# Kernel tuning notes

Measured on AMD Instinct MI355X. Metric: run time of the kernel, lower is better.

Reference implementation:

```python
import jax, jax.numpy as jnp
import numpy as np

B, IN, H, D, C, K = 4096, 128, 256, 32, 8, 256
HS = D // 2  # structure_filter hidden (latent_dim > 2)
EPS = 1e-6
MAX_NORM = 0.99


def _gelu(t):
    return jax.nn.gelu(t, approximate=False)  # torch nn.GELU default = exact erf


def _project_to_ball(z):
    norm = jnp.maximum(jnp.linalg.norm(z, axis=-1, keepdims=True), EPS)
    scale = jnp.minimum(MAX_NORM / norm, 1.0)
    return z * scale


def _hyperbolic_distance(xp, yp):
    # Poincare-ball distance: arccosh(1 + 2*|x-y|^2 / ((1-|x|^2)(1-|y|^2)))
    sq = jnp.sum((xp - yp) ** 2, axis=-1)
    xn = jnp.sum(xp * xp, axis=-1)
    yn = jnp.sum(yp * yp, axis=-1)
    denom = jnp.maximum((1.0 - xn) * (1.0 - yn), EPS)
    arg = jnp.maximum(1.0 + 2.0 * sq / denom, 1.0 + EPS)
    return jnp.arccosh(arg)


def setup_inputs() -> dict:
    key = jax.random.key(0)
    ks = jax.random.split(key, 14)
    n = lambda k, shape, s: (jax.random.normal(k, shape, dtype=jnp.float32) * s)
    centers = jax.random.normal(ks[7], (C, D), dtype=jnp.float32)
    centers = centers / jnp.maximum(jnp.linalg.norm(centers, axis=-1, keepdims=True), EPS)
    return {
        "x": jax.random.normal(ks[0], (B, IN), dtype=jnp.float32),
        "W1": n(ks[1], (IN, H), 0.05), "b1": jnp.zeros((H,), jnp.float32),
        "W2": n(ks[2], (H, H), 0.05), "b2": jnp.zeros((H,), jnp.float32),
        "Wv": n(ks[3], (H, D), 0.05), "bv": jnp.zeros((D,), jnp.float32),
        "centers": centers,
        "codebook": n(ks[8], (C, K, D), 0.02),
        "Ws1": n(ks[9], (D, HS), 0.1), "bs1": jnp.zeros((HS,), jnp.float32),
        "Ws2": n(ks[10], (HS, D), 0.1), "bs2": jnp.zeros((D,), jnp.float32),
    }


def reference(x, W1, b1, W2, b2, Wv, bv, centers, codebook, Ws1, bs1, Ws2, bs2):
    sg = jax.lax.stop_gradient
    feats = _gelu(_gelu(x @ W1 + b1) @ W2 + b2)          # [B,H]
    v = feats @ Wv + bv                                   # [B,D]
    scores = (v @ centers.T) / jnp.sqrt(jnp.asarray(D, v.dtype))
    router = jax.nn.softmax(scores, axis=-1)              # [B,C]
    K_chart = jnp.argmax(router, axis=1)                  # [B]
    c_bar = router @ centers                              # [B,D]
    v_local = v - c_bar                                   # [B,D]
    diff = v_local[:, None, None, :] - codebook[None]     # [B,C,K,D]
    dist = jnp.sum(diff * diff, axis=-1)                  # [B,C,K]
    indices = jnp.argmin(dist, axis=-1)                   # [B,C]
    z_q_all = codebook[jnp.arange(C)[None, :], indices]   # [B,C,D]
    v_bc = jnp.broadcast_to(v_local[:, None, :], z_q_all.shape)
    v_proj = _project_to_ball(v_bc)
    w_det = sg(router)
    d_cb = _hyperbolic_distance(z_q_all, sg(v_proj))      # [B,C]
    codebook_loss = jnp.sum(jnp.mean(d_cb ** 2 * w_det, axis=0))
    d_cm = _hyperbolic_distance(sg(z_q_all), v_proj)
    commitment = jnp.sum(jnp.mean(d_cm ** 2 * w_det, axis=0))
    vq_loss = codebook_loss + 0.25 * commitment
    z_q_blended = jnp.sum(z_q_all * router[..., None], axis=1)  # [B,D]
    K_code = jnp.take_along_axis(indices, K_chart[:, None], axis=1)[:, 0]
    delta = v_local[:, None, :] - sg(z_q_all)             # [B,C,D]
    z_n_all = _gelu(delta @ Ws1 + bs1) @ Ws2 + bs2        # [B,C,D]
    z_n = jnp.sum(z_n_all * router[..., None], axis=1)    # [B,D]
    z_tex = (v_local - sg(z_q_blended)) - z_n
    z_q_st = v_local + sg(z_q_blended - v_local)
    z_geo = c_bar + z_q_st + z_n
    return (K_chart, K_code, z_n, z_tex, router, z_geo, vq_loss, indices, z_n_all, c_bar, v_local)
```

## Files before the change

### kernel.cpp

```cpp
#include <hip/hip_runtime.h>
#include <math.h>

#define NB 4096
#define NIN 128
#define NH 256
#define ND 32
#define NC 8
#define NK 256
#define NHS 16

#define OFF_KCHART 0
#define OFF_KCODE  4096
#define OFF_ZN     8192
#define OFF_ZTEX   (OFF_ZN + 4096*32)
#define OFF_ROUTER (OFF_ZTEX + 4096*32)
#define OFF_ZGEO   (OFF_ROUTER + 4096*8)
#define OFF_LOSS   (OFF_ZGEO + 4096*32)
#define OFF_IND    (OFF_LOSS + 1)
#define OFF_ZNALL  (OFF_IND + 4096*8)
#define OFF_CBAR   (OFF_ZNALL + 4096*8*32)
#define OFF_VLOC   (OFF_CBAR + 4096*32)

__device__ __forceinline__ float gelu_exact(float x) {
    return x * (erff(x / 1.41421356237309504f) + 1.0f) * 0.5f;
}

template<int K>
__global__ __launch_bounds__(256)
void gemm_bias_gelu(const float* __restrict__ A, const float* __restrict__ W,
                    const float* __restrict__ bias, float* __restrict__ out) {
    const int N = 256;
    __shared__ float sB[2][32][68];
    const int t  = threadIdx.x;
    const int n0 = blockIdx.x * 64;
    const int r0 = blockIdx.y * 32;
    const int ty = t >> 4, tx = t & 15;
    const int bk = t >> 4, bc = t & 15;

    float4 bias4 = *(const float4*)(bias + n0 + tx * 4);

    float4 pb0 = *(const float4*)(W + bk * N + n0 + bc * 4);
    float4 pb1 = *(const float4*)(W + (bk + 16) * N + n0 + bc * 4);

    const float* Ab0 = A + (r0 + ty * 2 + 0) * K;
    const float* Ab1 = A + (r0 + ty * 2 + 1) * K;
    float ac[2][4], an[2][4];
    {
        float4 c0 = *(const float4*)(Ab0 + 0), c1 = *(const float4*)(Ab1 + 0);
        ac[0][0]=c0.x; ac[0][1]=c0.y; ac[0][2]=c0.z; ac[0][3]=c0.w;
        ac[1][0]=c1.x; ac[1][1]=c1.y; ac[1][2]=c1.z; ac[1][3]=c1.w;
        float4 d0 = *(const float4*)(Ab0 + 4), d1 = *(const float4*)(Ab1 + 4);
        an[0][0]=d0.x; an[0][1]=d0.y; an[0][2]=d0.z; an[0][3]=d0.w;
        an[1][0]=d1.x; an[1][1]=d1.y; an[1][2]=d1.z; an[1][3]=d1.w;
    }

    float acc[2][4];
    #pragma unroll
    for (int i = 0; i < 2; i++)
        #pragma unroll
        for (int j = 0; j < 4; j++) acc[i][j] = 0.f;

    int buf = 0;
    for (int kk = 0; kk < K; kk += 32) {
        *(float4*)(&sB[buf][bk][bc*4])    = pb0;
        *(float4*)(&sB[buf][bk+16][bc*4]) = pb1;
        __syncthreads();
        if (kk + 32 < K) {
            pb0 = *(const float4*)(W + (kk + 32 + bk) * N + n0 + bc * 4);
            pb1 = *(const float4*)(W + (kk + 32 + bk + 16) * N + n0 + bc * 4);
        }
        #pragma unroll
        for (int c = 0; c < 8; c++) {
            int knext = kk + (c + 2) * 4;
            if (knext > K - 4) knext = K - 4;
            float4 p0 = *(const float4*)(Ab0 + knext);
            float4 p1 = *(const float4*)(Ab1 + knext);
            #pragma unroll
            for (int u = 0; u < 4; u++) {
                float4 bv = *(const float4*)(&sB[buf][c * 4 + u][tx * 4]);
                float bb[4] = {bv.x, bv.y, bv.z, bv.w};
                #pragma unroll
                for (int j = 0; j < 4; j++) {
                    acc[0][j] = fmaf(ac[0][u], bb[j], acc[0][j]);
                    acc[1][j] = fmaf(ac[1][u], bb[j], acc[1][j]);
                }
            }
            #pragma unroll
            for (int u = 0; u < 4; u++) { ac[0][u] = an[0][u]; ac[1][u] = an[1][u]; }
            an[0][0]=p0.x; an[0][1]=p0.y; an[0][2]=p0.z; an[0][3]=p0.w;
            an[1][0]=p1.x; an[1][1]=p1.y; an[1][2]=p1.z; an[1][3]=p1.w;
        }
        buf ^= 1;
    }
    float bb4[4] = {bias4.x, bias4.y, bias4.z, bias4.w};
    #pragma unroll
    for (int i = 0; i < 2; i++) {
        int row = r0 + ty * 2 + i;
        float4 o;
        float* op = (float*)&o;
        #pragma unroll
        for (int j = 0; j < 4; j++) op[j] = gelu_exact(acc[i][j] + bb4[j]);
        *(float4*)(out + row * N + n0 + tx * 4) = o;
    }
}

__global__ __launch_bounds__(256)
void router_kernel(const float* __restrict__ feats, const float* __restrict__ Wv,
                   const float* __restrict__ bv, const float* __restrict__ centers,
                   float* __restrict__ out, float* __restrict__ vloc_ws) {
    __shared__ float sWvT[ND][260];
    __shared__ float sCent[NC * ND];
    __shared__ float sV[8][ND + 2];
    __shared__ float sScore[8][NC];
    __shared__ float sRout[8][NC];
    const int t = threadIdx.x;
    const int row0 = blockIdx.x * 8;
    {
        #pragma unroll
        for (int q = 0; q < 8; q++) {
            int id = t + q * 256;
            int k = id >> 3, c4 = (id & 7) * 4;
            float4 w = ((const float4*)Wv)[id];
            sWvT[c4 + 0][k] = w.x;
            sWvT[c4 + 1][k] = w.y;
            sWvT[c4 + 2][k] = w.z;
            sWvT[c4 + 3][k] = w.w;
        }
        if (t < 64) ((float4*)sCent)[t] = ((const float4*)centers)[t];
    }
    __syncthreads();
    const int r = t >> 5, cp = t & 31;
    const int row = row0 + r;
    float a0 = bv[cp];
    const float4* f4 = (const float4*)(feats + row * NH);
    for (int k4 = 0; k4 < NH / 4; k4++) {
        float4 f = f4[k4];
        float4 w = *(const float4*)(&sWvT[cp][k4 * 4]);
        a0 = fmaf(f.x, w.x, a0);
        a0 = fmaf(f.y, w.y, a0);
        a0 = fmaf(f.z, w.z, a0);
        a0 = fmaf(f.w, w.w, a0);
    }
    sV[r][cp] = a0;
    __syncthreads();
    if (t < 64) {
        int rr = t >> 3, c = t & 7;
        float s = 0.f;
        #pragma unroll
        for (int k = 0; k < ND; k++) s = fmaf(sV[rr][k], sCent[c * ND + k], s);
        sScore[rr][c] = s / 5.65685424949238f;
    }
    __syncthreads();
    if (t < 8) {
        const int rr = t, grow = row0 + rr;
        float sc[NC];
        float m = -3.4e38f; int kmax = 0;
        #pragma unroll
        for (int c = 0; c < NC; c++) {
            float s = sScore[rr][c];
            sc[c] = s;
            if (s > m) { m = s; kmax = c; }
        }
        float ssum = 0.f;
        #pragma unroll
        for (int c = 0; c < NC; c++) { float e = expf(sc[c] - m); sc[c] = e; ssum += e; }
        float inv = 1.f / ssum;
        #pragma unroll
        for (int c = 0; c < NC; c++) {
            float rv = sc[c] * inv;
            sRout[rr][c] = rv;
            out[OFF_ROUTER + grow * NC + c] = rv;
        }
        out[OFF_KCHART + grow] = (float)kmax;
    }
    __syncthreads();
    {
        const int col = cp;
        float cb = 0.f;
        #pragma unroll
        for (int c = 0; c < NC; c++) cb = fmaf(sRout[r][c], sCent[c * ND + col], cb);
        float vl = sV[r][col] - cb;
        out[OFF_CBAR + row * ND + col] = cb;
        out[OFF_VLOC + row * ND + col] = vl;
        vloc_ws[row * ND + col] = vl;
    }
}

__global__ __launch_bounds__(256)
void vq_chart(const float* __restrict__ codebook, const float* __restrict__ vloc_ws,
              const float* __restrict__ Ws1, const float* __restrict__ bs1,
              const float* __restrict__ Ws2, const float* __restrict__ bs2,
              float* __restrict__ out, float* __restrict__ loss_partial) {
    __shared__ float sCB[NK][36];
    __shared__ float sEn2[NK];
    __shared__ float sV[64][36];
    __shared__ float sBest[8][64];
    __shared__ int   sBidx[8][64];
    __shared__ int   sSel[64];
    __shared__ float sRoutv[64];
    __shared__ float sPscale[64];
    __shared__ float sLossArr[64];
    __shared__ float sWs1[ND][17];
    __shared__ float sWs2[NHS][33];
    __shared__ float sbs1[NHS], sbs2v[ND];
    const int t = threadIdx.x;
    const int c = blockIdx.x & 7;
    const int row0 = (blockIdx.x >> 3) * 64;

    {
        const float4* src = (const float4*)(codebook + c * NK * ND);
        #pragma unroll
        for (int q = 0; q < 8; q++) {
            int id = t + q * 256;
            int code = id >> 3, kq = (id & 7) * 4;
            *(float4*)(&sCB[code][kq]) = src[id];
        }
        #pragma unroll
        for (int q = 0; q < 2; q++) {
            int id = t + q * 256;
            int rr = id >> 3, kq = (id & 7) * 4;
            *(float4*)(&sV[rr][kq]) = ((const float4*)(vloc_ws + row0 * ND))[id];
        }
    }
    if (t < 128) {
        float4 w = ((const float4*)Ws1)[t];
        int k = t >> 2, o = (t & 3) * 4;
        sWs1[k][o] = w.x; sWs1[k][o+1] = w.y; sWs1[k][o+2] = w.z; sWs1[k][o+3] = w.w;
    } else {
        int u = t - 128;
        float4 w = ((const float4*)Ws2)[u];
        int k = u >> 3, o = (u & 7) * 4;
        sWs2[k][o] = w.x; sWs2[k][o+1] = w.y; sWs2[k][o+2] = w.z; sWs2[k][o+3] = w.w;
    }
    if (t < NHS) sbs1[t] = bs1[t];
    else if (t < NHS + ND) sbs2v[t - NHS] = bs2[t - NHS];
    if (t < 64) sRoutv[t] = out[OFF_ROUTER + (row0 + t) * NC + c];
    __syncthreads();
    {
        float s = 0.f;
        #pragma unroll
        for (int q = 0; q < 8; q++) {
            float4 e = *(const float4*)(&sCB[t][q * 4]);
            s = fmaf(e.x, e.x, s); s = fmaf(e.y, e.y, s);
            s = fmaf(e.z, e.z, s); s = fmaf(e.w, e.w, s);
        }
        sEn2[t] = s;
    }
    __syncthreads();

    const int r = t & 31, g = t >> 5;
    float vl0[ND], vl1[ND];
    #pragma unroll
    for (int q = 0; q < 8; q++) {
        float4 a = *(const float4*)(&sV[r][q * 4]);
        vl0[q*4] = a.x; vl0[q*4+1] = a.y; vl0[q*4+2] = a.z; vl0[q*4+3] = a.w;
        float4 b = *(const float4*)(&sV[r + 32][q * 4]);
        vl1[q*4] = b.x; vl1[q*4+1] = b.y; vl1[q*4+2] = b.z; vl1[q*4+3] = b.w;
    }
    float best0 = 3.4e38f, best1 = 3.4e38f;
    int bi0 = 0, bi1 = 0;
    for (int j = 0; j < 32; j++) {
        const int code = g * 32 + j;
        float dot0 = 0.f, dot1 = 0.f;
        #pragma unroll
        for (int q = 0; q < 8; q++) {
            float4 e = *(const float4*)(&sCB[code][q * 4]);
            dot0 = fmaf(vl0[q*4+0], e.x, dot0); dot1 = fmaf(vl1[q*4+0], e.x, dot1);
            dot0 = fmaf(vl0[q*4+1], e.y, dot0); dot1 = fmaf(vl1[q*4+1], e.y, dot1);
            dot0 = fmaf(vl0[q*4+2], e.z, dot0); dot1 = fmaf(vl1[q*4+2], e.z, dot1);
            dot0 = fmaf(vl0[q*4+3], e.w, dot0); dot1 = fmaf(vl1[q*4+3], e.w, dot1);
        }
        const float en2 = sEn2[code];
        float d0 = en2 - 2.f * dot0;
        float d1 = en2 - 2.f * dot1;
        if (d0 < best0) { best0 = d0; bi0 = code; }
        if (d1 < best1) { best1 = d1; bi1 = code; }
    }
    sBest[g][r] = best0;      sBidx[g][r] = bi0;
    sBest[g][r + 32] = best1; sBidx[g][r + 32] = bi1;
    __syncthreads();
    if (t < 64) {
        float bb = sBest[0][t]; int ii = sBidx[0][t];
        #pragma unroll
        for (int gg = 1; gg < 8; gg++) {
            float v = sBest[gg][t];
            if (v < bb) { bb = v; ii = sBidx[gg][t]; }
        }
        sSel[t] = ii;
        out[OFF_IND + (row0 + t) * NC + c] = (float)ii;
        float vn2 = 0.f;
        #pragma unroll
        for (int k = 0; k < ND; k++) { float v = sV[t][k]; vn2 = fmaf(v, v, vn2); }
        float norm = fmaxf(sqrtf(vn2), 1e-6f);
        sPscale[t] = fminf(0.99f / norm, 1.0f);
    }
    __syncthreads();

    const int i = t & 15, r16 = t >> 4;
    const float b1r = sbs1[i];
    const float bo0 = sbs2v[2*i], bo1 = sbs2v[2*i+1];
    #pragma unroll
    for (int pass = 0; pass < 4; pass++) {
        const int lrow = pass * 16 + r16;
        const int grow = row0 + lrow;
        const int sel = sSel[lrow];
        const float rc = sRoutv[lrow];
        const float ps = sPscale[lrow];
        float acc1 = b1r;
        #pragma unroll
        for (int k = 0; k < ND; k++) {
            float dlt = sV[lrow][k] - sCB[sel][k];
            acc1 = fmaf(dlt, sWs1[k][i], acc1);
        }
        float h = gelu_exact(acc1);
        float a0 = bo0, a1 = bo1;
        #pragma unroll
        for (int k = 0; k < NHS; k++) {
            float s1k = __shfl(h, k, 16);
            a0 = fmaf(s1k, sWs2[k][2*i],   a0);
            a1 = fmaf(s1k, sWs2[k][2*i+1], a1);
        }
        out[OFF_ZNALL + (grow * NC + c) * ND + 2*i]     = a0;
        out[OFF_ZNALL + (grow * NC + c) * ND + 2*i + 1] = a1;
        const float e0 = sCB[sel][2*i], e1 = sCB[sel][2*i+1];
        float yp0 = sV[lrow][2*i] * ps, yp1 = sV[lrow][2*i+1] * ps;
        float d0 = e0 - yp0, d1 = e1 - yp1;
        float sq = fmaf(d0, d0, d1 * d1);
        float xn = fmaf(e0, e0, e1 * e1);
        float yn = fmaf(yp0, yp0, yp1 * yp1);
        #pragma unroll
        for (int m = 1; m < 16; m <<= 1) {
            sq += __shfl_xor(sq, m, 16);
            xn += __shfl_xor(xn, m, 16);
            yn += __shfl_xor(yn, m, 16);
        }
        if (i == 0) {
            float denom = fmaxf((1.f - xn) * (1.f - yn), 1e-6f);
            float arg = fmaxf(1.f + 2.f * sq / denom, 1.f + 1e-6f);
            float dd = acoshf(arg);
            sLossArr[lrow] = dd * dd * rc;
        }
    }
    __syncthreads();
    if (t < 64) {
        float v = sLossArr[t];
        #pragma unroll
        for (int off = 32; off > 0; off >>= 1) v += __shfl_down(v, off, 64);
        if (t == 0) loss_partial[blockIdx.x] = v;
    }
}

__global__ __launch_bounds__(256)
void finalize2_kernel(const float* __restrict__ codebook, const float* __restrict__ vloc_ws,
                      float* __restrict__ out, const float* __restrict__ partials) {
    const int gid = blockIdx.x * 256 + threadIdx.x;
    const int row = gid >> 5;
    const int col = gid & 31;
    float rout[NC]; int ind[NC];
    #pragma unroll
    for (int cc = 0; cc < NC; cc++) {
        rout[cc] = out[OFF_ROUTER + row * NC + cc];
        ind[cc]  = (int)out[OFF_IND + row * NC + cc];
    }
    float zn = 0.f, zq = 0.f;
    #pragma unroll
    for (int cc = 0; cc < NC; cc++) {
        const float rcc = rout[cc];
        zn = fmaf(out[OFF_ZNALL + (row * NC + cc) * ND + col], rcc, zn);
        zq = fmaf(codebook[(cc * NK + ind[cc]) * ND + col], rcc, zq);
    }
    const float vl = vloc_ws[row * ND + col];
    const float cb = out[OFF_CBAR + row * ND + col];
    out[OFF_ZN   + row * ND + col] = zn;
    out[OFF_ZTEX + row * ND + col] = vl - zq - zn;
    out[OFF_ZGEO + row * ND + col] = cb + zq + zn;
    if (col == 0) {
        int kc = (int)out[OFF_KCHART + row];
        out[OFF_KCODE + row] = out[OFF_IND + row * NC + kc];
    }
    if (blockIdx.x == 0) {
        __shared__ float sTmp[4];
        const int t = threadIdx.x;
        float v = partials[t] + partials[t + 256];
        #pragma unroll
        for (int off = 32; off > 0; off >>= 1) v += __shfl_down(v, off, 64);
        if ((t & 63) == 0) sTmp[t >> 6] = v;
        __syncthreads();
        if (t == 0) out[OFF_LOSS] = 1.25f * (sTmp[0] + sTmp[1] + sTmp[2] + sTmp[3]) / 4096.f;
    }
}

extern "C" void kernel_launch(void* const* d_in, const int* in_sizes, int n_in,
                              void* d_out, int out_size, void* d_ws, size_t ws_size,
                              hipStream_t stream) {
    const float* x        = (const float*)d_in[0];
    const float* W1       = (const float*)d_in[1];
    const float* b1       = (const float*)d_in[2];
    const float* W2       = (const float*)d_in[3];
    const float* b2       = (const float*)d_in[4];
    const float* Wv       = (const float*)d_in[5];
    const float* bv       = (const float*)d_in[6];
    const float* centers  = (const float*)d_in[7];
    const float* codebook = (const float*)d_in[8];
    const float* Ws1      = (const float*)d_in[9];
    const float* bs1      = (const float*)d_in[10];
    const float* Ws2      = (const float*)d_in[11];
    const float* bs2      = (const float*)d_in[12];
    float* out = (float*)d_out;
    float* ws  = (float*)d_ws;

    float* h1       = ws;
    float* feats    = ws + 4096 * 256;
    float* vloc     = ws + 2 * 4096 * 256;
    float* partials = ws + 2 * 4096 * 256 + 4096 * 32;

    gemm_bias_gelu<128><<<dim3(4, 128), dim3(256), 0, stream>>>(x, W1, b1, h1);
    gemm_bias_gelu<256><<<dim3(4, 128), dim3(256), 0, stream>>>(h1, W2, b2, feats);
    router_kernel<<<dim3(512), dim3(256), 0, stream>>>(feats, Wv, bv, centers, out, vloc);
    vq_chart<<<dim3(512), dim3(256), 0, stream>>>(codebook, vloc, Ws1, bs1, Ws2, bs2, out, partials);
    finalize2_kernel<<<dim3(512), dim3(256), 0, stream>>>(codebook, vloc, out, partials);
}
```

Before: 59.96 us.

## Fuse Wv projection into second GEMM epilogue and router into VQ kernel

```diff
diff --git a/kernel.cpp b/kernel.cpp
--- a/kernel.cpp
+++ b/kernel.cpp
@@ -38,7 +38,6 @@
     const int bk = t >> 4, bc = t & 15;
 
     float4 bias4 = *(const float4*)(bias + n0 + tx * 4);
-
     float4 pb0 = *(const float4*)(W + bk * N + n0 + bc * 4);
     float4 pb1 = *(const float4*)(W + (bk + 16) * N + n0 + bc * 4);
 
@@ -105,110 +104,135 @@
 }
 
 __global__ __launch_bounds__(256)
-void router_kernel(const float* __restrict__ feats, const float* __restrict__ Wv,
-                   const float* __restrict__ bv, const float* __restrict__ centers,
-                   float* __restrict__ out, float* __restrict__ vloc_ws) {
-    __shared__ float sWvT[ND][260];
-    __shared__ float sCent[NC * ND];
-    __shared__ float sV[8][ND + 2];
-    __shared__ float sScore[8][NC];
-    __shared__ float sRout[8][NC];
-    const int t = threadIdx.x;
-    const int row0 = blockIdx.x * 8;
+void gemm2_vproj(const float* __restrict__ A, const float* __restrict__ W,
+                 const float* __restrict__ bias, const float* __restrict__ Wv,
+                 float* __restrict__ vpart) {
+    const int K = 256, N = 256;
+    __shared__ float sB[2][32][68];
+    __shared__ float sWvT[32][68];
+    const int t  = threadIdx.x;
+    const int n0 = blockIdx.x * 64;
+    const int r0 = blockIdx.y * 32;
+    const int ty = t >> 4, tx = t & 15;
+    const int bk = t >> 4, bc = t & 15;
+
+    float4 bias4 = *(const float4*)(bias + n0 + tx * 4);
+    float4 pb0 = *(const float4*)(W + bk * N + n0 + bc * 4);
+    float4 pb1 = *(const float4*)(W + (bk + 16) * N + n0 + bc * 4);
+
+    const float* Ab0 = A + (r0 + ty * 2 + 0) * K;
+    const float* Ab1 = A + (r0 + ty * 2 + 1) * K;
+    float ac[2][4], an[2][4];
     {
-        #pragma unroll
-        for (int q = 0; q < 8; q++) {
-            int id = t + q * 256;
-            int k = id >> 3, c4 = (id & 7) * 4;
-            float4 w = ((const float4*)Wv)[id];
-            sWvT[c4 + 0][k] = w.x;
-            sWvT[c4 + 1][k] = w.y;
-            sWvT[c4 + 2][k] = w.z;
-            sWvT[c4 + 3][k] = w.w;
-        }
-        if (t < 64) ((float4*)sCent)[t] = ((const float4*)centers)[t];
-    }
-    __syncthreads();
-    const int r = t >> 5, cp = t & 31;
-    const int row = row0 + r;
-    float a0 = bv[cp];
-    const float4* f4 = (const float4*)(feats + row * NH);
-    for (int k4 = 0; k4 < NH / 4; k4++) {
-        float4 f = f4[k4];
-        float4 w = *(const float4*)(&sWvT[cp][k4 * 4]);
-        a0 = fmaf(f.x, w.x, a0);
-        a0 = fmaf(f.y, w.y, a0);
-        a0 = fmaf(f.z, w.z, a0);
-        a0 = fmaf(f.w, w.w, a0);
-    }
-    sV[r][cp] = a0;
-    __syncthreads();
-    if (t < 64) {
-        int rr = t >> 3, c = t & 7;
-        float s = 0.f;
-        #pragma unroll
-        for (int k = 0; k < ND; k++) s = fmaf(sV[rr][k], sCent[c * ND + k], s);
-        sScore[rr][c] = s / 5.65685424949238f;
-    }
-    __syncthreads();
-    if (t < 8) {
-        const int rr = t, grow = row0 + rr;
-        float sc[NC];
-        float m = -3.4e38f; int kmax = 0;
-        #pragma unroll
-        for (int c = 0; c < NC; c++) {
-            float s = sScore[rr][c];
-            sc[c] = s;
-            if (s > m) { m = s; kmax = c; }
-        }
-        float ssum = 0.f;
-        #pragma unroll
-        for (int c = 0; c < NC; c++) { float e = expf(sc[c] - m); sc[c] = e; ssum += e; }
-        float inv = 1.f / ssum;
-        #pragma unroll
-        for (int c = 0; c < NC; c++) {
-            float rv = sc[c] * inv;
-            sRout[rr][c] = rv;
-            out[OFF_ROUTER + grow * NC + c] = rv;
-        }
-        out[OFF_KCHART + grow] = (float)kmax;
-    }
-    __syncthreads();
+        float4 c0 = *(const float4*)(Ab0 + 0), c1 = *(const float4*)(Ab1 + 0);
+        ac[0][0]=c0.x; ac[0][1]=c0.y; ac[0][2]=c0.z; ac[0][3]=c0.w;
+        ac[1][0]=c1.x; ac[1][1]=c1.y; ac[1][2]=c1.z; ac[1][3]=c1.w;
+        float4 d0 = *(const float4*)(Ab0 + 4), d1 = *(const float4*)(Ab1 + 4);
+        an[0][0]=d0.x; an[0][1]=d0.y; an[0][2]=d0.z; an[0][3]=d0.w;
+        an[1][0]=d1.x; an[1][1]=d1.y; an[1][2]=d1.z; an[1][3]=d1.w;
+    }
+
+    float acc[2][4];
+    #pragma unroll
+    for (int i = 0; i < 2; i++)
+        #pragma unroll
+        for (int j = 0; j < 4; j++) acc[i][j] = 0.f;
+
+    int buf = 0;
+    for (int kk = 0; kk < K; kk += 32) {
+        *(float4*)(&sB[buf][bk][bc*4])    = pb0;
+        *(float4*)(&sB[buf][bk+16][bc*4]) = pb1;
+        __syncthreads();
+        if (kk + 32 < K) {
+            pb0 = *(const float4*)(W + (kk + 32 + bk) * N + n0 + bc * 4);
+            pb1 = *(const float4*)(W + (kk + 32 + bk + 16) * N + n0 + bc * 4);
+        }
+        #pragma unroll
+        for (int c = 0; c < 8; c++) {
+            int knext = kk + (c + 2) * 4;
+            if (knext > K - 4) knext = K - 4;
+            float4 p0 = *(const float4*)(Ab0 + knext);
+            float4 p1 = *(const float4*)(Ab1 + knext);
+            #pragma unroll
+            for (int u = 0; u < 4; u++) {
+                float4 bv = *(const float4*)(&sB[buf][c * 4 + u][tx * 4]);
+                float bb[4] = {bv.x, bv.y, bv.z, bv.w};
+                #pragma unroll
+                for (int j = 0; j < 4; j++) {
+                    acc[0][j] = fmaf(ac[0][u], bb[j], acc[0][j]);
+                    acc[1][j] = fmaf(ac[1][u], bb[j], acc[1][j]);
+                }
+            }
+            #pragma unroll
+            for (int u = 0; u < 4; u++) { ac[0][u] = an[0][u]; ac[1][u] = an[1][u]; }
+            an[0][0]=p0.x; an[0][1]=p0.y; an[0][2]=p0.z; an[0][3]=p0.w;
+            an[1][0]=p1.x; an[1][1]=p1.y; an[1][2]=p1.z; an[1][3]=p1.w;
+        }
+        buf ^= 1;
+    }
+    float f[2][4];
     {
-        const int col = cp;
-        float cb = 0.f;
-        #pragma unroll
-        for (int c = 0; c < NC; c++) cb = fmaf(sRout[r][c], sCent[c * ND + col], cb);
-        float vl = sV[r][col] - cb;
-        out[OFF_CBAR + row * ND + col] = cb;
-        out[OFF_VLOC + row * ND + col] = vl;
-        vloc_ws[row * ND + col] = vl;
+        float bb4[4] = {bias4.x, bias4.y, bias4.z, bias4.w};
+        #pragma unroll
+        for (int i = 0; i < 2; i++)
+            #pragma unroll
+            for (int j = 0; j < 4; j++) f[i][j] = gelu_exact(acc[i][j] + bb4[j]);
+    }
+    #pragma unroll
+    for (int q = 0; q < 2; q++) {
+        int id = t * 2 + q;
+        int kr = id >> 3, c4 = (id & 7) * 4;
+        float4 w = *(const float4*)(Wv + (n0 + kr) * ND + c4);
+        sWvT[c4+0][kr] = w.x; sWvT[c4+1][kr] = w.y;
+        sWvT[c4+2][kr] = w.z; sWvT[c4+3][kr] = w.w;
+    }
+    __syncthreads();
+    #pragma unroll
+    for (int c = 0; c < ND; c++) {
+        float4 w = *(const float4*)(&sWvT[c][tx * 4]);
+        float s0 = f[0][0] * w.x; s0 = fmaf(f[0][1], w.y, s0);
+        s0 = fmaf(f[0][2], w.z, s0); s0 = fmaf(f[0][3], w.w, s0);
+        float s1 = f[1][0] * w.x; s1 = fmaf(f[1][1], w.y, s1);
+        s1 = fmaf(f[1][2], w.z, s1); s1 = fmaf(f[1][3], w.w, s1);
+        s0 += __shfl_down(s0, 8, 16); s1 += __shfl_down(s1, 8, 16);
+        s0 += __shfl_down(s0, 4, 16); s1 += __shfl_down(s1, 4, 16);
+        s0 += __shfl_down(s0, 2, 16); s1 += __shfl_down(s1, 2, 16);
+        s0 += __shfl_down(s0, 1, 16); s1 += __shfl_down(s1, 1, 16);
+        if (tx == 0) {
+            vpart[blockIdx.x * (NB * ND) + (r0 + ty * 2 + 0) * ND + c] = s0;
+            vpart[blockIdx.x * (NB * ND) + (r0 + ty * 2 + 1) * ND + c] = s1;
+        }
     }
 }
 
 __global__ __launch_bounds__(256)
-void vq_chart(const float* __restrict__ codebook, const float* __restrict__ vloc_ws,
+void vq_chart(const float* __restrict__ codebook, const float* __restrict__ centers,
+              const float* __restrict__ bvp, const float* __restrict__ vpart,
               const float* __restrict__ Ws1, const float* __restrict__ bs1,
               const float* __restrict__ Ws2, const float* __restrict__ bs2,
-              float* __restrict__ out, float* __restrict__ loss_partial) {
+              float* __restrict__ out, float* __restrict__ vloc_ws,
+              float* __restrict__ loss_partial) {
     __shared__ float sCB[NK][36];
     __shared__ float sEn2[NK];
     __shared__ float sV[64][36];
+    __shared__ float sCent[NC * ND];
+    __shared__ float sbv[ND];
+    __shared__ float sScore[64][NC + 1];
+    __shared__ float sRout[64][NC + 1];
     __shared__ float sBest[8][64];
     __shared__ int   sBidx[8][64];
     __shared__ int   sSel[64];
-    __shared__ float sRoutv[64];
     __shared__ float sPscale[64];
     __shared__ float sLossArr[64];
     __shared__ float sWs1[ND][17];
     __shared__ float sWs2[NHS][33];
     __shared__ float sbs1[NHS], sbs2v[ND];
     const int t = threadIdx.x;
-    const int c = blockIdx.x & 7;
+    const int cblk = blockIdx.x & 7;
     const int row0 = (blockIdx.x >> 3) * 64;
 
     {
-        const float4* src = (const float4*)(codebook + c * NK * ND);
+        const float4* src = (const float4*)(codebook + cblk * NK * ND);
         #pragma unroll
         for (int q = 0; q < 8; q++) {
             int id = t + q * 256;
@@ -218,8 +242,26 @@
         #pragma unroll
         for (int q = 0; q < 2; q++) {
             int id = t + q * 256;
-            int rr = id >> 3, kq = (id & 7) * 4;
-            *(float4*)(&sV[rr][kq]) = ((const float4*)(vloc_ws + row0 * ND))[id];
+            int rr = id >> 3, c4 = id & 7;
+            const float4* p0 = (const float4*)(vpart + 0 * (NB * ND) + (row0 + rr) * ND);
+            const float4* p1 = (const float4*)(vpart + 1 * (NB * ND) + (row0 + rr) * ND);
+            const float4* p2 = (const float4*)(vpart + 2 * (NB * ND) + (row0 + rr) * ND);
+            const float4* p3 = (const float4*)(vpart + 3 * (NB * ND) + (row0 + rr) * ND);
+            float4 a = p0[c4], b = p1[c4], cc = p2[c4], d = p3[c4];
+            float4 bb = ((const float4*)bvp)[c4];
+            float4 v;
+            v.x = a.x + b.x + cc.x + d.x + bb.x;
+            v.y = a.y + b.y + cc.y + d.y + bb.y;
+            v.z = a.z + b.z + cc.z + d.z + bb.z;
+            v.w = a.w + b.w + cc.w + d.w + bb.w;
+            *(float4*)(&sV[rr][c4 * 4]) = v;
+        }
+    }
+    if (t < 64) ((float4*)sCent)[t] = ((const float4*)centers)[t];
+    if (t >= 64 && t < 72) ((float4*)sbv)[t - 64] = ((const float4*)bvp)[t - 64];
+    if (t >= 128 && t < 256) {
+        int u = t - 128;
+        if (u < 64) {
         }
     }
     if (t < 128) {
@@ -234,13 +276,72 @@
     }
     if (t < NHS) sbs1[t] = bs1[t];
     else if (t < NHS + ND) sbs2v[t - NHS] = bs2[t - NHS];
-    if (t < 64) sRoutv[t] = out[OFF_ROUTER + (row0 + t) * NC + c];
-    __syncthreads();
+    __syncthreads();
+
     {
+        const int r = t >> 2, cp = t & 3;
+        float4 vr[8];
+        #pragma unroll
+        for (int q = 0; q < 8; q++) vr[q] = *(const float4*)(&sV[r][q * 4]);
+        #pragma unroll
+        for (int cc = 0; cc < 2; cc++) {
+            int ch = cp * 2 + cc;
+            float s = 0.f;
+            #pragma unroll
+            for (int q = 0; q < 8; q++) {
+                float4 ce = *(const float4*)(&sCent[ch * ND + q * 4]);
+                s = fmaf(vr[q].x, ce.x, s);
+                s = fmaf(vr[q].y, ce.y, s);
+                s = fmaf(vr[q].z, ce.z, s);
+                s = fmaf(vr[q].w, ce.w, s);
+            }
+            sScore[r][ch] = s / 5.65685424949238f;
+        }
+    }
+    __syncthreads();
+    if (t < 64) {
+        const int r = t, grow = row0 + r;
+        float sc[NC];
+        float m = -3.4e38f; int kmax = 0;
+        #pragma unroll
+        for (int c = 0; c < NC; c++) {
+            float s = sScore[r][c];
+            sc[c] = s;
+            if (s > m) { m = s; kmax = c; }
+        }
+        float ssum = 0.f;
+        #pragma unroll
+        for (int c = 0; c < NC; c++) { float e = expf(sc[c] - m); sc[c] = e; ssum += e; }
+        float inv = 1.f / ssum;
+        #pragma unroll
+        for (int c = 0; c < NC; c++) {
+            float rv = sc[c] * inv;
+            sRout[r][c] = rv;
+            if (cblk == 0) out[OFF_ROUTER + grow * NC + c] = rv;
+        }
+        if (cblk == 0) out[OFF_KCHART + grow] = (float)kmax;
+    }
+    __syncthreads();
+    {
+        const int r = t >> 2, q = t & 3;
+        #pragma unroll
+        for (int u = 0; u < 8; u++) {
+            int col = q * 8 + u;
+            float cb = 0.f;
+            #pragma unroll
+            for (int c = 0; c < NC; c++) cb = fmaf(sRout[r][c], sCent[c * ND + col], cb);
+            float vl = sV[r][col] - cb;
+            sV[r][col] = vl;
+            if (cblk == 0) {
+                out[OFF_CBAR + (row0 + r) * ND + col] = cb;
+                out[OFF_VLOC + (row0 + r) * ND + col] = vl;
+                vloc_ws[(row0 + r) * ND + col] = vl;
+            }
+        }
         float s = 0.f;
         #pragma unroll
-        for (int q = 0; q < 8; q++) {
-            float4 e = *(const float4*)(&sCB[t][q * 4]);
+        for (int qq = 0; qq < 8; qq++) {
+            float4 e = *(const float4*)(&sCB[t][qq * 4]);
             s = fmaf(e.x, e.x, s); s = fmaf(e.y, e.y, s);
             s = fmaf(e.z, e.z, s); s = fmaf(e.w, e.w, s);
         }
@@ -287,7 +388,7 @@
             if (v < bb) { bb = v; ii = sBidx[gg][t]; }
         }
         sSel[t] = ii;
-        out[OFF_IND + (row0 + t) * NC + c] = (float)ii;
+        out[OFF_IND + (row0 + t) * NC + cblk] = (float)ii;
         float vn2 = 0.f;
         #pragma unroll
         for (int k = 0; k < ND; k++) { float v = sV[t][k]; vn2 = fmaf(v, v, vn2); }
@@ -304,7 +405,7 @@
         const int lrow = pass * 16 + r16;
         const int grow = row0 + lrow;
         const int sel = sSel[lrow];
-        const float rc = sRoutv[lrow];
+        const float rc = sRout[lrow][cblk];
         const float ps = sPscale[lrow];
         float acc1 = b1r;
         #pragma unroll
@@ -320,8 +421,8 @@
             a0 = fmaf(s1k, sWs2[k][2*i],   a0);
             a1 = fmaf(s1k, sWs2[k][2*i+1], a1);
         }
-        out[OFF_ZNALL + (grow * NC + c) * ND + 2*i]     = a0;
-        out[OFF_ZNALL + (grow * NC + c) * ND + 2*i + 1] = a1;
+        out[OFF_ZNALL + (grow * NC + cblk) * ND + 2*i]     = a0;
+        out[OFF_ZNALL + (grow * NC + cblk) * ND + 2*i + 1] = a1;
         const float e0 = sCB[sel][2*i], e1 = sCB[sel][2*i+1];
         float yp0 = sV[lrow][2*i] * ps, yp1 = sV[lrow][2*i+1] * ps;
         float d0 = e0 - yp0, d1 = e1 - yp1;
@@ -409,14 +510,14 @@
     float* out = (float*)d_out;
     float* ws  = (float*)d_ws;
 
-    float* h1       = ws;
-    float* feats    = ws + 4096 * 256;
-    float* vloc     = ws + 2 * 4096 * 256;
-    float* partials = ws + 2 * 4096 * 256 + 4096 * 32;
+    float* h1    = ws;
+    float* vpart = ws + 4096 * 256;
+    float* vloc  = ws + 4096 * 256 + 4 * 4096 * 32;
+    float* lpart = ws + 4096 * 256 + 5 * 4096 * 32;
 
     gemm_bias_gelu<128><<<dim3(4, 128), dim3(256), 0, stream>>>(x, W1, b1, h1);
-    gemm_bias_gelu<256><<<dim3(4, 128), dim3(256), 0, stream>>>(h1, W2, b2, feats);
-    router_kernel<<<dim3(512), dim3(256), 0, stream>>>(feats, Wv, bv, centers, out, vloc);
-    vq_chart<<<dim3(512), dim3(256), 0, stream>>>(codebook, vloc, Ws1, bs1, Ws2, bs2, out, partials);
-    finalize2_kernel<<<dim3(512), dim3(256), 0, stream>>>(codebook, vloc, out, partials);
+    gemm2_vproj<<<dim3(4, 128), dim3(256), 0, stream>>>(h1, W2, b2, Wv, vpart);
+    vq_chart<<<dim3(512), dim3(256), 0, stream>>>(codebook, centers, bv, vpart,
+                                                  Ws1, bs1, Ws2, bs2, out, vloc, lpart);
+    finalize2_kernel<<<dim3(512), dim3(256), 0, stream>>>(codebook, vloc, out, lpart);
 }
```

After: 67.62 us. 12.8% more time.

## Enlarge GEMM row tiles and restructure VQ search and MLP register reuse

Applied to the files above, without the earlier changes.

```diff
diff --git a/kernel.cpp b/kernel.cpp
--- a/kernel.cpp
+++ b/kernel.cpp
@@ -33,7 +33,7 @@
     __shared__ float sB[2][32][68];
     const int t  = threadIdx.x;
     const int n0 = blockIdx.x * 64;
-    const int r0 = blockIdx.y * 32;
+    const int r0 = blockIdx.y * 64;
     const int ty = t >> 4, tx = t & 15;
     const int bk = t >> 4, bc = t & 15;
 
@@ -42,21 +42,29 @@
     float4 pb0 = *(const float4*)(W + bk * N + n0 + bc * 4);
     float4 pb1 = *(const float4*)(W + (bk + 16) * N + n0 + bc * 4);
 
-    const float* Ab0 = A + (r0 + ty * 2 + 0) * K;
-    const float* Ab1 = A + (r0 + ty * 2 + 1) * K;
-    float ac[2][4], an[2][4];
+    const float* Ab0 = A + (r0 + ty * 4 + 0) * K;
+    const float* Ab1 = A + (r0 + ty * 4 + 1) * K;
+    const float* Ab2 = A + (r0 + ty * 4 + 2) * K;
+    const float* Ab3 = A + (r0 + ty * 4 + 3) * K;
+    float ac[4][4], an[4][4];
     {
         float4 c0 = *(const float4*)(Ab0 + 0), c1 = *(const float4*)(Ab1 + 0);
+        float4 c2 = *(const float4*)(Ab2 + 0), c3 = *(const float4*)(Ab3 + 0);
         ac[0][0]=c0.x; ac[0][1]=c0.y; ac[0][2]=c0.z; ac[0][3]=c0.w;
         ac[1][0]=c1.x; ac[1][1]=c1.y; ac[1][2]=c1.z; ac[1][3]=c1.w;
-        float4 d0 = *(const float4*)(Ab0 + 4), d1 = *(const float4*)(Ab1 + 4);
-        an[0][0]=d0.x; an[0][1]=d0.y; an[0][2]=d0.z; an[0][3]=d0.w;
-        an[1][0]=d1.x; an[1][1]=d1.y; an[1][2]=d1.z; an[1][3]=d1.w;
-    }
-
-    float acc[2][4];
-    #pragma unroll
-    for (int i = 0; i < 2; i++)
+        ac[2][0]=c2.x; ac[2][1]=c2.y; ac[2][2]=c2.z; ac[2][3]=c2.w;
+        ac[3][0]=c3.x; ac[3][1]=c3.y; ac[3][2]=c3.z; ac[3][3]=c3.w;
+        float4 n0v = *(const float4*)(Ab0 + 4), n1v = *(const float4*)(Ab1 + 4);
+        float4 n2v = *(const float4*)(Ab2 + 4), n3v = *(const float4*)(Ab3 + 4);
+        an[0][0]=n0v.x; an[0][1]=n0v.y; an[0][2]=n0v.z; an[0][3]=n0v.w;
+        an[1][0]=n1v.x; an[1][1]=n1v.y; an[1][2]=n1v.z; an[1][3]=n1v.w;
+        an[2][0]=n2v.x; an[2][1]=n2v.y; an[2][2]=n2v.z; an[2][3]=n2v.w;
+        an[3][0]=n3v.x; an[3][1]=n3v.y; an[3][2]=n3v.z; an[3][3]=n3v.w;
+    }
+
+    float acc[4][4];
+    #pragma unroll
+    for (int i = 0; i < 4; i++)
         #pragma unroll
         for (int j = 0; j < 4; j++) acc[i][j] = 0.f;
 
@@ -75,6 +83,8 @@
             if (knext > K - 4) knext = K - 4;
             float4 p0 = *(const float4*)(Ab0 + knext);
             float4 p1 = *(const float4*)(Ab1 + knext);
+            float4 p2 = *(const float4*)(Ab2 + knext);
+            float4 p3 = *(const float4*)(Ab3 + knext);
             #pragma unroll
             for (int u = 0; u < 4; u++) {
                 float4 bv = *(const float4*)(&sB[buf][c * 4 + u][tx * 4]);
@@ -83,19 +93,26 @@
                 for (int j = 0; j < 4; j++) {
                     acc[0][j] = fmaf(ac[0][u], bb[j], acc[0][j]);
                     acc[1][j] = fmaf(ac[1][u], bb[j], acc[1][j]);
+                    acc[2][j] = fmaf(ac[2][u], bb[j], acc[2][j]);
+                    acc[3][j] = fmaf(ac[3][u], bb[j], acc[3][j]);
                 }
             }
             #pragma unroll
-            for (int u = 0; u < 4; u++) { ac[0][u] = an[0][u]; ac[1][u] = an[1][u]; }
+            for (int u = 0; u < 4; u++) {
+                ac[0][u] = an[0][u]; ac[1][u] = an[1][u];
+                ac[2][u] = an[2][u]; ac[3][u] = an[3][u];
+            }
             an[0][0]=p0.x; an[0][1]=p0.y; an[0][2]=p0.z; an[0][3]=p0.w;
             an[1][0]=p1.x; an[1][1]=p1.y; an[1][2]=p1.z; an[1][3]=p1.w;
+            an[2][0]=p2.x; an[2][1]=p2.y; an[2][2]=p2.z; an[2][3]=p2.w;
+            an[3][0]=p3.x; an[3][1]=p3.y; an[3][2]=p3.z; an[3][3]=p3.w;
         }
         buf ^= 1;
     }
     float bb4[4] = {bias4.x, bias4.y, bias4.z, bias4.w};
     #pragma unroll
-    for (int i = 0; i < 2; i++) {
-        int row = r0 + ty * 2 + i;
+    for (int i = 0; i < 4; i++) {
+        int row = r0 + ty * 4 + i;
         float4 o;
         float* op = (float*)&o;
         #pragma unroll
@@ -186,7 +203,7 @@
     }
 }
 
-__global__ __launch_bounds__(256)
+__global__ __launch_bounds__(256, 2)
 void vq_chart(const float* __restrict__ codebook, const float* __restrict__ vloc_ws,
               const float* __restrict__ Ws1, const float* __restrict__ bs1,
               const float* __restrict__ Ws2, const float* __restrict__ bs2,
@@ -194,14 +211,14 @@
     __shared__ float sCB[NK][36];
     __shared__ float sEn2[NK];
     __shared__ float sV[64][36];
-    __shared__ float sBest[8][64];
-    __shared__ int   sBidx[8][64];
+    __shared__ float sBest[16][64];
+    __shared__ int   sBidx[16][64];
     __shared__ int   sSel[64];
     __shared__ float sRoutv[64];
     __shared__ float sPscale[64];
     __shared__ float sLossArr[64];
-    __shared__ float sWs1[ND][17];
-    __shared__ float sWs2[NHS][33];
+    __shared__ float sWs1T[NHS][36];
+    __shared__ float sWs2T[ND][20];
     __shared__ float sbs1[NHS], sbs2v[ND];
     const int t = threadIdx.x;
     const int c = blockIdx.x & 7;
@@ -225,12 +242,14 @@
     if (t < 128) {
         float4 w = ((const float4*)Ws1)[t];
         int k = t >> 2, o = (t & 3) * 4;
-        sWs1[k][o] = w.x; sWs1[k][o+1] = w.y; sWs1[k][o+2] = w.z; sWs1[k][o+3] = w.w;
+        sWs1T[o+0][k] = w.x; sWs1T[o+1][k] = w.y;
+        sWs1T[o+2][k] = w.z; sWs1T[o+3][k] = w.w;
     } else {
         int u = t - 128;
         float4 w = ((const float4*)Ws2)[u];
         int k = u >> 3, o = (u & 7) * 4;
-        sWs2[k][o] = w.x; sWs2[k][o+1] = w.y; sWs2[k][o+2] = w.z; sWs2[k][o+3] = w.w;
+        sWs2T[o+0][k] = w.x; sWs2T[o+1][k] = w.y;
+        sWs2T[o+2][k] = w.z; sWs2T[o+3][k] = w.w;
     }
     if (t < NHS) sbs1[t] = bs1[t];
     else if (t < NHS + ND) sbs2v[t - NHS] = bs2[t - NHS];
@@ -248,43 +267,56 @@
     }
     __syncthreads();
 
-    const int r = t & 31, g = t >> 5;
-    float vl0[ND], vl1[ND];
-    #pragma unroll
-    for (int q = 0; q < 8; q++) {
-        float4 a = *(const float4*)(&sV[r][q * 4]);
-        vl0[q*4] = a.x; vl0[q*4+1] = a.y; vl0[q*4+2] = a.z; vl0[q*4+3] = a.w;
-        float4 b = *(const float4*)(&sV[r + 32][q * 4]);
-        vl1[q*4] = b.x; vl1[q*4+1] = b.y; vl1[q*4+2] = b.z; vl1[q*4+3] = b.w;
-    }
-    float best0 = 3.4e38f, best1 = 3.4e38f;
-    int bi0 = 0, bi1 = 0;
-    for (int j = 0; j < 32; j++) {
-        const int code = g * 32 + j;
-        float dot0 = 0.f, dot1 = 0.f;
-        #pragma unroll
-        for (int q = 0; q < 8; q++) {
-            float4 e = *(const float4*)(&sCB[code][q * 4]);
-            dot0 = fmaf(vl0[q*4+0], e.x, dot0); dot1 = fmaf(vl1[q*4+0], e.x, dot1);
-            dot0 = fmaf(vl0[q*4+1], e.y, dot0); dot1 = fmaf(vl1[q*4+1], e.y, dot1);
-            dot0 = fmaf(vl0[q*4+2], e.z, dot0); dot1 = fmaf(vl1[q*4+2], e.z, dot1);
-            dot0 = fmaf(vl0[q*4+3], e.w, dot0); dot1 = fmaf(vl1[q*4+3], e.w, dot1);
-        }
-        const float en2 = sEn2[code];
-        float d0 = en2 - 2.f * dot0;
-        float d1 = en2 - 2.f * dot1;
-        if (d0 < best0) { best0 = d0; bi0 = code; }
-        if (d1 < best1) { best1 = d1; bi1 = code; }
-    }
-    sBest[g][r] = best0;      sBidx[g][r] = bi0;
-    sBest[g][r + 32] = best1; sBidx[g][r + 32] = bi1;
+    {
+        const int r = t & 15, g = t >> 4;
+        float vl[4][ND];
+        #pragma unroll
+        for (int u = 0; u < 4; u++) {
+            #pragma unroll
+            for (int q = 0; q < 8; q++) {
+                float4 a = *(const float4*)(&sV[r + u * 16][q * 4]);
+                vl[u][q*4] = a.x; vl[u][q*4+1] = a.y;
+                vl[u][q*4+2] = a.z; vl[u][q*4+3] = a.w;
+            }
+        }
+        float best[4] = {3.4e38f, 3.4e38f, 3.4e38f, 3.4e38f};
+        int bi[4] = {0, 0, 0, 0};
+        for (int j = 0; j < 16; j++) {
+            const int code = g * 16 + ((j + g * 4) & 15);
+            float dot[4] = {0.f, 0.f, 0.f, 0.f};
+            #pragma unroll
+            for (int q = 0; q < 8; q++) {
+                float4 e = *(const float4*)(&sCB[code][q * 4]);
+                #pragma unroll
+                for (int u = 0; u < 4; u++) {
+                    dot[u] = fmaf(vl[u][q*4+0], e.x, dot[u]);
+                    dot[u] = fmaf(vl[u][q*4+1], e.y, dot[u]);
+                    dot[u] = fmaf(vl[u][q*4+2], e.z, dot[u]);
+                    dot[u] = fmaf(vl[u][q*4+3], e.w, dot[u]);
+                }
+            }
+            const float en2 = sEn2[code];
+            #pragma unroll
+            for (int u = 0; u < 4; u++) {
+                float d = en2 - 2.f * dot[u];
+                if (d < best[u] || (d == best[u] && code < bi[u])) {
+                    best[u] = d; bi[u] = code;
+                }
+            }
+        }
+        #pragma unroll
+        for (int u = 0; u < 4; u++) {
+            sBest[g][r + u * 16] = best[u];
+            sBidx[g][r + u * 16] = bi[u];
+        }
+    }
     __syncthreads();
     if (t < 64) {
         float bb = sBest[0][t]; int ii = sBidx[0][t];
         #pragma unroll
-        for (int gg = 1; gg < 8; gg++) {
-            float v = sBest[gg][t];
-            if (v < bb) { bb = v; ii = sBidx[gg][t]; }
+        for (int gg = 1; gg < 16; gg++) {
+            float v = sBest[gg][t]; int id = sBidx[gg][t];
+            if (v < bb || (v == bb && id < ii)) { bb = v; ii = id; }
         }
         sSel[t] = ii;
         out[OFF_IND + (row0 + t) * NC + c] = (float)ii;
@@ -299,6 +331,19 @@
     const int i = t & 15, r16 = t >> 4;
     const float b1r = sbs1[i];
     const float bo0 = sbs2v[2*i], bo1 = sbs2v[2*i+1];
+    float w1c[ND], w2a[NHS], w2b[NHS];
+    #pragma unroll
+    for (int q = 0; q < 8; q++) {
+        float4 w = *(const float4*)(&sWs1T[i][q * 4]);
+        w1c[q*4] = w.x; w1c[q*4+1] = w.y; w1c[q*4+2] = w.z; w1c[q*4+3] = w.w;
+    }
+    #pragma unroll
+    for (int q = 0; q < 4; q++) {
+        float4 a = *(const float4*)(&sWs2T[2*i][q * 4]);
+        w2a[q*4] = a.x; w2a[q*4+1] = a.y; w2a[q*4+2] = a.z; w2a[q*4+3] = a.w;
+        float4 b = *(const float4*)(&sWs2T[2*i+1][q * 4]);
+        w2b[q*4] = b.x; w2b[q*4+1] = b.y; w2b[q*4+2] = b.z; w2b[q*4+3] = b.w;
+    }
     #pragma unroll
     for (int pass = 0; pass < 4; pass++) {
         const int lrow = pass * 16 + r16;
@@ -306,19 +351,24 @@
         const int sel = sSel[lrow];
         const float rc = sRoutv[lrow];
         const float ps = sPscale[lrow];
+        float dta[ND];
+        #pragma unroll
+        for (int q = 0; q < 8; q++) {
+            float4 vv = *(const float4*)(&sV[lrow][q * 4]);
+            float4 ee = *(const float4*)(&sCB[sel][q * 4]);
+            dta[q*4+0] = vv.x - ee.x; dta[q*4+1] = vv.y - ee.y;
+            dta[q*4+2] = vv.z - ee.z; dta[q*4+3] = vv.w - ee.w;
+        }
         float acc1 = b1r;
         #pragma unroll
-        for (int k = 0; k < ND; k++) {
-            float dlt = sV[lrow][k] - sCB[sel][k];
-            acc1 = fmaf(dlt, sWs1[k][i], acc1);
-        }
+        for (int k = 0; k < ND; k++) acc1 = fmaf(dta[k], w1c[k], acc1);
         float h = gelu_exact(acc1);
         float a0 = bo0, a1 = bo1;
         #pragma unroll
         for (int k = 0; k < NHS; k++) {
             float s1k = __shfl(h, k, 16);
-            a0 = fmaf(s1k, sWs2[k][2*i],   a0);
-            a1 = fmaf(s1k, sWs2[k][2*i+1], a1);
+            a0 = fmaf(s1k, w2a[k], a0);
+            a1 = fmaf(s1k, w2b[k], a1);
         }
         out[OFF_ZNALL + (grow * NC + c) * ND + 2*i]     = a0;
         out[OFF_ZNALL + (grow * NC + c) * ND + 2*i + 1] = a1;
@@ -414,8 +464,8 @@
     float* vloc     = ws + 2 * 4096 * 256;
     float* partials = ws + 2 * 4096 * 256 + 4096 * 32;
 
-    gemm_bias_gelu<128><<<dim3(4, 128), dim3(256), 0, stream>>>(x, W1, b1, h1);
-    gemm_bias_gelu<256><<<dim3(4, 128), dim3(256), 0, stream>>>(h1, W2, b2, feats);
+    gemm_bias_gelu<128><<<dim3(4, 64), dim3(256), 0, stream>>>(x, W1, b1, h1);
+    gemm_bias_gelu<256><<<dim3(4, 64), dim3(256), 0, stream>>>(h1, W2, b2, feats);
     router_kernel<<<dim3(512), dim3(256), 0, stream>>>(feats, Wv, bv, centers, out, vloc);
     vq_chart<<<dim3(512), dim3(256), 0, stream>>>(codebook, vloc, Ws1, bs1, Ws2, bs2, out, partials);
     finalize2_kernel<<<dim3(512), dim3(256), 0, stream>>>(codebook, vloc, out, partials);
```

After: 65.24 us. 8.8% more time.
